# Performance work log

Measured on AMD Instinct MI355X. Metric: run time of the kernel, lower is better.

Reference implementation:

```python
import jax, jax.numpy as jnp
import numpy as np

BETA = 0.5

def setup_inputs() -> dict:
    key = jax.random.key(0)
    ks = jax.random.split(key, 12)
    B, H, d, hid = 2048, 100, 128, 256
    item_num, region_num, dist_num = 100000, 1000, 16
    return {
        "history": jax.random.randint(ks[0], (B, H), 0, item_num),
        "target": jax.random.randint(ks[1], (B,), 0, item_num),
        "history_region": jax.random.randint(ks[2], (B, H), 0, region_num),
        "target_region": jax.random.randint(ks[3], (B,), 0, region_num),
        "target_distance": jax.random.uniform(ks[4], (B,), dtype=jnp.float32),
        "E_hist": jax.random.normal(ks[5], (item_num, d), dtype=jnp.float32) * 0.01,
        "E_tgt": jax.random.normal(ks[6], (item_num, d), dtype=jnp.float32) * 0.01,
        "E_reg": jax.random.normal(ks[7], (region_num, d), dtype=jnp.float32) * 0.01,
        "E_dist": jax.random.normal(ks[8], (dist_num, d), dtype=jnp.float32) * 0.01,
        "W1": jax.random.normal(ks[9], (hid, 2 * d), dtype=jnp.float32) * 0.05,
        "b1": jnp.zeros((hid,), dtype=jnp.float32),
        "w2": jax.random.normal(ks[10], (hid,), dtype=jnp.float32) * 0.05,
    }

def reference(history, target, history_region, target_region, target_distance,
              E_hist, E_tgt, E_reg, E_dist, W1, b1, w2):
    # history embeddings: [B,H,2d]
    hist = jnp.concatenate([E_hist[history], E_reg[history_region]], axis=-1)
    # target embeddings: [B,1,2d]
    tgt = jnp.concatenate([E_tgt[target], E_reg[target_region]], axis=-1)[:, None, :]
    x = hist * tgt                                   # [B,H,2d]
    a = jax.nn.relu(jnp.einsum('bhd,kd->bhk', x, W1) + b1)  # [B,H,hid]
    score = jnp.einsum('bhk,k->bh', a, w2)           # [B,H]
    # distance bias: scalar per batch element
    dist = jnp.sum(target_distance[:, None] * E_dist[0], axis=1)  # [B]
    exp_A = jnp.exp(score + dist[:, None])           # [B,H]
    mask = (history != target[:, None]).astype(exp_A.dtype)
    exp_A = exp_A * mask
    exp_sum = jnp.power(jnp.sum(exp_A, axis=-1), BETA)  # [B]
    attn = exp_A / exp_sum[:, None]                  # [B,H]
    # weighted inner product: sum_h sum_d attn*hist*tgt
    pred = jnp.sum(hist * attn[:, :, None] * tgt, axis=(1, 2))  # [B]
    return jax.nn.sigmoid(pred)
```

## Files before the change

### kernel.cpp

```cpp
#include <hip/hip_runtime.h>
#include <stdint.h>

typedef __attribute__((ext_vector_type(8))) short bf16x8;
typedef __attribute__((ext_vector_type(4))) float f32x4;

#define HH  100
#define DD  128
#define HID 256
#define NT  7
#define NE  4

__device__ __forceinline__ unsigned short f2bf(float f) {
    unsigned int u = __float_as_uint(f);
    u += 0x7fffu + ((u >> 16) & 1u);
    return (unsigned short)(u >> 16);
}

__global__ void w1_pack(const float* __restrict__ W1, unsigned short* __restrict__ W1p) {
    int unit = blockIdx.x * 256 + threadIdx.x;
    int lane = unit & 63;
    int s    = (unit >> 6) & 7;
    int st   = unit >> 9;
    int col  = lane & 15, quad = lane >> 4;
    const float* src = W1 + (size_t)(st * 16 + col) * HID + s * 32 + quad * 8;
    union { unsigned short u[8]; bf16x8 v; } o;
    #pragma unroll
    for (int j = 0; j < 8; j++) o.u[j] = f2bf(src[j]);
    *(bf16x8*)(W1p + (size_t)unit * 8) = o.v;
}

__device__ __forceinline__ unsigned int cvt_pk_bf16(float lo, float hi) {
    unsigned int r;
    asm("v_cvt_pk_bf16_f32 %0, %1, %2" : "=v"(r) : "v"(lo), "v"(hi));
    return r;
}

#define CONSUME(V0, V1, S, AP, TGT, ACC) do {                                     \
    const float* tp_ = (TGT) + (S) * 32 + quad * 8;                               \
    float4 t0_ = *(const float4*)tp_, t1_ = *(const float4*)(tp_ + 4);            \
    float x0=(V0).x*t0_.x, x1=(V0).y*t0_.y, x2=(V0).z*t0_.z, x3=(V0).w*t0_.w;     \
    float x4=(V1).x*t1_.x, x5=(V1).y*t1_.y, x6=(V1).z*t1_.z, x7=(V1).w*t1_.w;     \
    (ACC) += (x0+x1)+(x2+x3)+((x4+x5)+(x6+x7));                                   \
    union { unsigned int u[4]; int4 v; } fb_;                                     \
    fb_.u[0]=cvt_pk_bf16(x0,x1); fb_.u[1]=cvt_pk_bf16(x2,x3);                     \
    fb_.u[2]=cvt_pk_bf16(x4,x5); fb_.u[3]=cvt_pk_bf16(x6,x7);                     \
    *(int4*)((AP) + (size_t)((S) * 64 + lane) * 8) = fb_.v;                       \
} while (0)

__global__ __launch_bounds__(256, 2) void nais_kernel(
    const int* __restrict__ history,
    const int* __restrict__ target,
    const int* __restrict__ history_region,
    const int* __restrict__ target_region,
    const float* __restrict__ target_distance,
    const float* __restrict__ E_hist,
    const float* __restrict__ E_tgt,
    const float* __restrict__ E_reg,
    const float* __restrict__ E_dist,
    const float* __restrict__ b1,
    const float* __restrict__ w2,
    const unsigned short* __restrict__ W1p,
    float* __restrict__ out,
    int Btot)
{
    __shared__ __align__(16) unsigned short As[NT * 4096];
    __shared__ __align__(16) float tgts[HID];
    __shared__ __align__(16) float b1s[HID];
    __shared__ __align__(16) float w2s[HID];
    __shared__ __align__(16) float scorep[4][112];
    __shared__ __align__(16) float xsum[112];
    __shared__ __align__(16) int   hidx2[2][HH];
    __shared__ __align__(16) int   hreg[HH];
    __shared__ float s_sumE;

    const int t    = threadIdx.x;
    const int lane = t & 63;
    const int wave = t >> 6;
    const int col  = lane & 15;
    const int quad = lane >> 4;

    const int base = blockIdx.x * NE;

    if (blockIdx.x * 2 >= gridDim.x) __builtin_amdgcn_s_sleep(80);

    if (wave == 3) {
        *(float4*)(b1s + lane * 4) = *(const float4*)(b1 + lane * 4);
        *(float4*)(w2s + lane * 4) = *(const float4*)(w2 + lane * 4);
    }
    if (wave == 1) {
        float v = E_dist[lane] + E_dist[64 + lane];
        #pragma unroll
        for (int off = 32; off; off >>= 1) v += __shfl_xor(v, off);
        if (lane == 0) s_sumE = v;
    }

    bf16x8 w1f[32];
    #pragma unroll
    for (int j = 0; j < 32; j++) {
        const int unit = ((wave * 4 + (j >> 3)) * 8 + (j & 7)) * 64 + lane;
        w1f[j] = *(const bf16x8*)(W1p + (size_t)unit * 8);
    }
    #pragma unroll
    for (int j = 0; j < 32; j++) asm volatile("" : "+a"(w1f[j]));

    __syncthreads();

    f32x4 bbv[4], wwv[4];
    #pragma unroll
    for (int st = 0; st < 4; st++) {
        bbv[st] = *(const f32x4*)&b1s[(wave * 4 + st) * 16 + quad * 4];
        wwv[st] = *(const f32x4*)&w2s[(wave * 4 + st) * 16 + quad * 4];
    }

    #pragma unroll 1
    for (int e = 0; e < NE; e++) {
        const int b = base + e;
        if (b >= Btot) break;

        const int   tg    = target[b];
        const float tdist = target_distance[b];
        int* hB = &hidx2[e & 1][0];

        if (t < HH) {
            hB[t]   = history[b * HH + t];
            hreg[t] = history_region[b * HH + t];
        }
        if (wave == 2) {
            float4 v;
            if (lane < 32) v = *(const float4*)(E_tgt + (size_t)tg * DD + lane * 4);
            else           v = *(const float4*)(E_reg + (size_t)target_region[b] * DD + (lane - 32) * 4);
            *(float4*)(tgts + lane * 4) = v;
        }
        __syncthreads();

        #pragma unroll 1
        for (int ti = 0; ti < 2; ti++) {
            const int tile = wave + ti * 4;
            if (tile >= NT) break;
            const int row = tile * 16 + col;
            const int rc  = (row < HH) ? row : row - 64;
            const int ih  = hB[rc];
            const int ir  = hreg[rc];
            const float* ph = E_hist + (size_t)ih * DD + quad * 8;
            const float* pr = E_reg  + (size_t)ir * DD + quad * 8;
            unsigned short* ap = &As[tile * 4096];
            float4 g[16];
            #pragma unroll
            for (int s = 0; s < 4; s++) {
                g[2*s]     = *(const float4*)(ph + s * 32);
                g[2*s + 1] = *(const float4*)(ph + s * 32 + 4);
                g[8 + 2*s] = *(const float4*)(pr + s * 32);
                g[9 + 2*s] = *(const float4*)(pr + s * 32 + 4);
            }
            float acc = 0.f;
            #pragma unroll
            for (int s = 0; s < 8; s++) CONSUME(g[2*s], g[2*s+1], s, ap, tgts, acc);
            float v = acc;
            v += __shfl_xor(v, 16);
            v += __shfl_xor(v, 32);
            if (quad == 0) xsum[row] = v;
        }
        __syncthreads();

        #pragma unroll 1
        for (int i = 0; i < NT; i++) {
            int mt = wave * 2 + i; if (mt >= NT) mt -= NT;
            const unsigned short* ap = &As[mt * 4096];
            f32x4 c0 = {0,0,0,0}, c1 = {0,0,0,0}, c2 = {0,0,0,0}, c3 = {0,0,0,0};
            #pragma unroll
            for (int s = 0; s < 8; s++) {
                bf16x8 xf = *(const bf16x8*)(ap + (size_t)(s * 64 + lane) * 8);
                c0 = __builtin_amdgcn_mfma_f32_16x16x32_bf16(w1f[s],      xf, c0, 0, 0, 0);
                c1 = __builtin_amdgcn_mfma_f32_16x16x32_bf16(w1f[8 + s],  xf, c1, 0, 0, 0);
                c2 = __builtin_amdgcn_mfma_f32_16x16x32_bf16(w1f[16 + s], xf, c2, 0, 0, 0);
                c3 = __builtin_amdgcn_mfma_f32_16x16x32_bf16(w1f[24 + s], xf, c3, 0, 0, 0);
            }
            float sp = 0.f;
            #pragma unroll
            for (int r = 0; r < 4; r++) {
                sp = fmaf(fmaxf(c0[r] + bbv[0][r], 0.f), wwv[0][r], sp);
                sp = fmaf(fmaxf(c1[r] + bbv[1][r], 0.f), wwv[1][r], sp);
                sp = fmaf(fmaxf(c2[r] + bbv[2][r], 0.f), wwv[2][r], sp);
                sp = fmaf(fmaxf(c3[r] + bbv[3][r], 0.f), wwv[3][r], sp);
            }
            sp += __shfl_xor(sp, 16);
            sp += __shfl_xor(sp, 32);
            if (quad == 0) scorep[wave][mt * 16 + col] = sp;
        }
        __syncthreads();

        if (wave == 0) {
            const float dist = tdist * s_sumE;
            float s1 = 0.f, s2 = 0.f;
            #pragma unroll
            for (int hh = 0; hh < 2; hh++) {
                const int h = lane + hh * 64;
                if (h < HH) {
                    float sc = scorep[0][h] + scorep[1][h] + scorep[2][h] + scorep[3][h];
                    if (hB[h] != tg) {
                        float ev = expf(sc + dist);
                        s1 += ev;
                        s2 += ev * xsum[h];
                    }
                }
            }
            #pragma unroll
            for (int off = 32; off; off >>= 1) {
                s1 += __shfl_xor(s1, off);
                s2 += __shfl_xor(s2, off);
            }
            if (lane == 0) {
                float pred = s2 / sqrtf(s1);
                out[b] = 1.f / (1.f + expf(-pred));
            }
        }
    }
}

extern "C" void kernel_launch(void* const* d_in, const int* in_sizes, int n_in,
                              void* d_out, int out_size, void* d_ws, size_t ws_size,
                              hipStream_t stream) {
    const int*   history         = (const int*)d_in[0];
    const int*   target          = (const int*)d_in[1];
    const int*   history_region  = (const int*)d_in[2];
    const int*   target_region   = (const int*)d_in[3];
    const float* target_distance = (const float*)d_in[4];
    const float* E_hist          = (const float*)d_in[5];
    const float* E_tgt           = (const float*)d_in[6];
    const float* E_reg           = (const float*)d_in[7];
    const float* E_dist          = (const float*)d_in[8];
    const float* W1              = (const float*)d_in[9];
    const float* b1              = (const float*)d_in[10];
    const float* w2              = (const float*)d_in[11];

    unsigned short* W1p = (unsigned short*)d_ws;
    const int B = in_sizes[1];

    const int grid = (B + NE - 1) / NE;

    w1_pack<<<32, 256, 0, stream>>>(W1, W1p);
    nais_kernel<<<grid, 256, 0, stream>>>(history, target, history_region, target_region,
                                          target_distance, E_hist, E_tgt, E_reg, E_dist,
                                          b1, w2, W1p, (float*)d_out, B);
}
```

Baseline: 210.2 us.

## Prefetch all per-block indices upfront and overlap next gather with softmax epilogue

Loads history indices, regions, targets and target embeddings for all NE batch elements once in the prologue. The gather and bf16 pack for element e+1 now runs in the same phase as the softmax epilogue of element e, and the work is split so wave 0 gathers one tile while the other waves gather two. This removes one barrier phase and the serialized index loads per element. It also drops the staggered s_sleep, moves W1 fragments from AGPR to VGPR constraints, and doubles xsum buffering, which may raise register pressure.

```diff
diff --git a/kernel.cpp b/kernel.cpp
--- a/kernel.cpp
+++ b/kernel.cpp
@@ -45,6 +45,31 @@
     fb_.u[0]=cvt_pk_bf16(x0,x1); fb_.u[1]=cvt_pk_bf16(x2,x3);                     \
     fb_.u[2]=cvt_pk_bf16(x4,x5); fb_.u[3]=cvt_pk_bf16(x6,x7);                     \
     *(int4*)((AP) + (size_t)((S) * 64 + lane) * 8) = fb_.v;                       \
+} while (0)
+
+#define GATHER_TILE(TILE, MS, XB) do {                                            \
+    const int row_ = (TILE) * 16 + col;                                           \
+    const int rc_  = (row_ < HH) ? row_ : row_ - 64;                              \
+    const int ih_  = hidx4[MS][rc_];                                              \
+    const int ir_  = hreg4[MS][rc_];                                              \
+    const float* ph_ = E_hist + (size_t)ih_ * DD + quad * 8;                      \
+    const float* pr_ = E_reg  + (size_t)ir_ * DD + quad * 8;                      \
+    unsigned short* ap_ = &As[(TILE) * 4096];                                     \
+    float4 g_[16];                                                                \
+    _Pragma("unroll")                                                             \
+    for (int s_ = 0; s_ < 4; s_++) {                                              \
+        g_[2*s_]     = *(const float4*)(ph_ + s_ * 32);                           \
+        g_[2*s_ + 1] = *(const float4*)(ph_ + s_ * 32 + 4);                       \
+        g_[8 + 2*s_] = *(const float4*)(pr_ + s_ * 32);                           \
+        g_[9 + 2*s_] = *(const float4*)(pr_ + s_ * 32 + 4);                       \
+    }                                                                             \
+    float acc_ = 0.f;                                                             \
+    _Pragma("unroll")                                                             \
+    for (int s_ = 0; s_ < 8; s_++) CONSUME(g_[2*s_], g_[2*s_+1], s_, ap_, &tgts4[MS][0], acc_); \
+    float v_ = acc_;                                                              \
+    v_ += __shfl_xor(v_, 16);                                                     \
+    v_ += __shfl_xor(v_, 32);                                                     \
+    if (quad == 0) xsum2[XB][row_] = v_;                                          \
 } while (0)
 
 __global__ __launch_bounds__(256, 2) void nais_kernel(
@@ -64,13 +89,15 @@
     int Btot)
 {
     __shared__ __align__(16) unsigned short As[NT * 4096];
-    __shared__ __align__(16) float tgts[HID];
+    __shared__ __align__(16) float tgts4[NE][HID];
     __shared__ __align__(16) float b1s[HID];
     __shared__ __align__(16) float w2s[HID];
     __shared__ __align__(16) float scorep[4][112];
-    __shared__ __align__(16) float xsum[112];
-    __shared__ __align__(16) int   hidx2[2][HH];
-    __shared__ __align__(16) int   hreg[HH];
+    __shared__ __align__(16) float xsum2[2][112];
+    __shared__ __align__(16) int   hidx4[NE][HH];
+    __shared__ __align__(16) int   hreg4[NE][HH];
+    __shared__ int   tgA[NE];
+    __shared__ float tdA[NE];
     __shared__ float s_sumE;
 
     const int t    = threadIdx.x;
@@ -80,9 +107,14 @@
     const int quad = lane >> 4;
 
     const int base = blockIdx.x * NE;
-
-    if (blockIdx.x * 2 >= gridDim.x) __builtin_amdgcn_s_sleep(80);
-
+    int cnt = Btot - base;
+    if (cnt <= 0) return;
+    if (cnt > NE) cnt = NE;
+
+    if (t < cnt) {
+        tgA[t] = target[base + t];
+        tdA[t] = target_distance[base + t];
+    }
     if (wave == 3) {
         *(float4*)(b1s + lane * 4) = *(const float4*)(b1 + lane * 4);
         *(float4*)(w2s + lane * 4) = *(const float4*)(w2 + lane * 4);
@@ -93,6 +125,21 @@
         for (int off = 32; off; off >>= 1) v += __shfl_xor(v, off);
         if (lane == 0) s_sumE = v;
     }
+    if (wave < cnt) {
+        const int tg2 = target[base + wave];
+        const int tr2 = target_region[base + wave];
+        float4 v;
+        if (lane < 32) v = *(const float4*)(E_tgt + (size_t)tg2 * DD + lane * 4);
+        else           v = *(const float4*)(E_reg + (size_t)tr2 * DD + (lane - 32) * 4);
+        *(float4*)(&tgts4[wave][lane * 4]) = v;
+    }
+    #pragma unroll
+    for (int e = 0; e < NE; e++) {
+        if (e < cnt && t < HH) {
+            hidx4[e][t] = history[(size_t)(base + e) * HH + t];
+            hreg4[e][t] = history_region[(size_t)(base + e) * HH + t];
+        }
+    }
 
     bf16x8 w1f[32];
     #pragma unroll
@@ -101,7 +148,7 @@
         w1f[j] = *(const bf16x8*)(W1p + (size_t)unit * 8);
     }
     #pragma unroll
-    for (int j = 0; j < 32; j++) asm volatile("" : "+a"(w1f[j]));
+    for (int j = 0; j < 32; j++) asm volatile("" : "+v"(w1f[j]));
 
     __syncthreads();
 
@@ -112,56 +159,15 @@
         wwv[st] = *(const f32x4*)&w2s[(wave * 4 + st) * 16 + quad * 4];
     }
 
+    if (wave == 0) { GATHER_TILE(0, 0, 0); }
+    else {
+        GATHER_TILE(wave, 0, 0);
+        GATHER_TILE(wave + 3, 0, 0);
+    }
+    __syncthreads();
+
     #pragma unroll 1
-    for (int e = 0; e < NE; e++) {
-        const int b = base + e;
-        if (b >= Btot) break;
-
-        const int   tg    = target[b];
-        const float tdist = target_distance[b];
-        int* hB = &hidx2[e & 1][0];
-
-        if (t < HH) {
-            hB[t]   = history[b * HH + t];
-            hreg[t] = history_region[b * HH + t];
-        }
-        if (wave == 2) {
-            float4 v;
-            if (lane < 32) v = *(const float4*)(E_tgt + (size_t)tg * DD + lane * 4);
-            else           v = *(const float4*)(E_reg + (size_t)target_region[b] * DD + (lane - 32) * 4);
-            *(float4*)(tgts + lane * 4) = v;
-        }
-        __syncthreads();
-
-        #pragma unroll 1
-        for (int ti = 0; ti < 2; ti++) {
-            const int tile = wave + ti * 4;
-            if (tile >= NT) break;
-            const int row = tile * 16 + col;
-            const int rc  = (row < HH) ? row : row - 64;
-            const int ih  = hB[rc];
-            const int ir  = hreg[rc];
-            const float* ph = E_hist + (size_t)ih * DD + quad * 8;
-            const float* pr = E_reg  + (size_t)ir * DD + quad * 8;
-            unsigned short* ap = &As[tile * 4096];
-            float4 g[16];
-            #pragma unroll
-            for (int s = 0; s < 4; s++) {
-                g[2*s]     = *(const float4*)(ph + s * 32);
-                g[2*s + 1] = *(const float4*)(ph + s * 32 + 4);
-                g[8 + 2*s] = *(const float4*)(pr + s * 32);
-                g[9 + 2*s] = *(const float4*)(pr + s * 32 + 4);
-            }
-            float acc = 0.f;
-            #pragma unroll
-            for (int s = 0; s < 8; s++) CONSUME(g[2*s], g[2*s+1], s, ap, tgts, acc);
-            float v = acc;
-            v += __shfl_xor(v, 16);
-            v += __shfl_xor(v, 32);
-            if (quad == 0) xsum[row] = v;
-        }
-        __syncthreads();
-
+    for (int e = 0; e < cnt; e++) {
         #pragma unroll 1
         for (int i = 0; i < NT; i++) {
             int mt = wave * 2 + i; if (mt >= NT) mt -= NT;
@@ -189,18 +195,22 @@
         }
         __syncthreads();
 
+        const bool gg = (e + 1 < cnt);
+        const int  nb = (e + 1) & 1;
         if (wave == 0) {
-            const float dist = tdist * s_sumE;
+            if (gg) { GATHER_TILE(0, e + 1, nb); }
+            const float dist = tdA[e] * s_sumE;
+            const int   tg   = tgA[e];
             float s1 = 0.f, s2 = 0.f;
             #pragma unroll
             for (int hh = 0; hh < 2; hh++) {
                 const int h = lane + hh * 64;
                 if (h < HH) {
                     float sc = scorep[0][h] + scorep[1][h] + scorep[2][h] + scorep[3][h];
-                    if (hB[h] != tg) {
+                    if (hidx4[e][h] != tg) {
                         float ev = expf(sc + dist);
                         s1 += ev;
-                        s2 += ev * xsum[h];
+                        s2 += ev * xsum2[e & 1][h];
                     }
                 }
             }
@@ -211,9 +221,13 @@
             }
             if (lane == 0) {
                 float pred = s2 / sqrtf(s1);
-                out[b] = 1.f / (1.f + expf(-pred));
-            }
+                out[base + e] = 1.f / (1.f + expf(-pred));
+            }
+        } else if (gg) {
+            GATHER_TILE(wave, e + 1, nb);
+            GATHER_TILE(wave + 3, e + 1, nb);
         }
+        __syncthreads();
     }
 }
 
```

Result: faster. 179.6 us (-14.5%).
